# Kernel tuning notes

Hardware: AMD Instinct MI355X
Metric: run time of the kernel (lower is better)

Reference implementation:

```python
import jax, jax.numpy as jnp
import numpy as np

EPS = 1e-5  # torch BatchNorm2d default


def _conv(x, w, padding):
    return jax.lax.conv_general_dilated(
        x, w, window_strides=(1, 1),
        padding=[(padding, padding), (padding, padding)],
        dimension_numbers=("NCHW", "OIHW", "NCHW"))


def _bn(x, gamma, beta):
    # training-mode batchnorm (biased variance), matching nn.BatchNorm2d forward
    mu = x.mean(axis=(0, 2, 3), keepdims=True)
    var = x.var(axis=(0, 2, 3), keepdims=True)
    xn = (x - mu) * jax.lax.rsqrt(var + EPS)
    return gamma[None, :, None, None] * xn + beta[None, :, None, None]


def _ste(x):
    # forward: sign(x); backward: pass gradient where |x| <= 1 (STE)
    m = (jnp.abs(x) <= 1.0).astype(x.dtype)
    s = jax.lax.stop_gradient(jnp.sign(x))
    return s + m * x - jax.lax.stop_gradient(m * x)


def _binconv(x, w, alpha, padding=1):
    # XNOR-style: sign both operands, full-precision conv, scale by alpha
    return _conv(jnp.sign(x), jnp.sign(w), padding) * alpha


def _maxpool2(x):
    return jax.lax.reduce_window(x, -jnp.inf, jax.lax.max,
                                 (1, 1, 2, 2), (1, 1, 2, 2), "VALID")


def setup_inputs() -> dict:
    key = jax.random.key(0)
    ks = jax.random.split(key, 8)

    def kaiming(k, shape):
        fan_out = shape[0] * shape[2] * shape[3]
        std = np.sqrt(2.0 / fan_out)
        return jax.random.normal(k, shape, dtype=jnp.float32) * std

    return {
        "x": jax.random.normal(ks[0], (128, 1, 128, 128), dtype=jnp.float32),
        # first conv (full precision) 1->32, k=3, pad=1
        "w1": kaiming(ks[1], (32, 1, 3, 3)),
        "b1": jnp.zeros((32,), jnp.float32),
        "g1": jnp.ones((32,), jnp.float32),
        "beta1": jnp.zeros((32,), jnp.float32),
        # BinaryConv2d 32->32
        "w2": kaiming(ks[2], (32, 32, 3, 3)),
        "a2": jnp.ones((1,), jnp.float32),
        "g2": jnp.ones((32,), jnp.float32),
        "beta2": jnp.zeros((32,), jnp.float32),
        # BinaryConv2d 32->64
        "w3": kaiming(ks[3], (64, 32, 3, 3)),
        "a3": jnp.ones((1,), jnp.float32),
        "g3": jnp.ones((64,), jnp.float32),
        "beta3": jnp.zeros((64,), jnp.float32),
        # BinaryConv2d 64->128
        "w4": kaiming(ks[4], (128, 64, 3, 3)),
        "a4": jnp.ones((1,), jnp.float32),
        # classifier 128->10
        "wf": jax.random.normal(ks[5], (10, 128), dtype=jnp.float32) * (1.0 / np.sqrt(128.0)),
        "bf": jnp.zeros((10,), jnp.float32),
    }


def reference(x, w1, b1, g1, beta1, w2, a2, g2, beta2, w3, a3, g3, beta3, w4, a4, wf, bf):
    h = _conv(x, w1, padding=1) + b1[None, :, None, None]   # [N,32,128,128]
    h = _bn(h, g1, beta1)
    h = _ste(h)
    h = _binconv(h, w2, a2)                                 # [N,32,128,128]
    h = _maxpool2(h)                                        # [N,32,64,64]
    h = _bn(h, g2, beta2)
    h = _ste(h)
    h = _binconv(h, w3, a3)                                 # [N,64,64,64]
    h = _maxpool2(h)                                        # [N,64,32,32]
    h = _bn(h, g3, beta3)
    h = _ste(h)
    h = _binconv(h, w4, a4)                                 # [N,128,32,32]
    h = h.mean(axis=(2, 3))                                 # AdaptiveAvgPool2d(1) -> [N,128]
    return h @ wf.T + bf                                    # [N,10]
```

## Files before the change

kernel.cpp:

```cpp
#include <hip/hip_runtime.h>
#include <stdint.h>
#include <limits.h>

constexpr int NB = 128;

__global__ void pack_weights_kernel(const float* __restrict__ w, uint32_t* __restrict__ out,
                                    int OC, int ICW)
{
    int idx = blockIdx.x * blockDim.x + threadIdx.x;
    int total = OC * 9 * ICW;
    if (idx >= total) return;
    int iw = idx % ICW;
    int t  = (idx / ICW) % 9;
    int oc = idx / (9 * ICW);
    int IC = ICW * 32;
    uint32_t word = 0;
    for (int b = 0; b < 32; ++b) {
        float wv = w[(size_t)(oc * IC + (iw * 32 + b)) * 9 + t];
        word |= (wv > 0.f ? 1u : 0u) << b;
    }
    out[idx] = word;
}

__global__ void zero_kernel(uint32_t* __restrict__ p, int n)
{
    int i = blockIdx.x * blockDim.x + threadIdx.x;
    int stride = gridDim.x * blockDim.x;
    for (; i < n; i += stride) p[i] = 0u;
}

__device__ __forceinline__ void conv1_load9(const float* __restrict__ x, int p, float* xv)
{
    int n = p >> 14;
    int y = (p >> 7) & 127;
    int c = p & 127;
    const float* xn = x + (size_t)n * 16384;
    #pragma unroll
    for (int ky = 0; ky < 3; ++ky)
    #pragma unroll
    for (int kx = 0; kx < 3; ++kx) {
        int yy = y + ky - 1, cc = c + kx - 1;
        float v = 0.f;
        if (yy >= 0 && yy < 128 && cc >= 0 && cc < 128) v = xn[yy * 128 + cc];
        xv[ky * 3 + kx] = v;
    }
}

__global__ __launch_bounds__(256) void xcorr_kernel(const float* __restrict__ x,
                                                    float* __restrict__ partials)
{
    __shared__ float wbuf[4][64];
    int tid = threadIdx.x;
    float s[9], c[45];
    #pragma unroll
    for (int t = 0; t < 9; ++t) s[t] = 0.f;
    #pragma unroll
    for (int q = 0; q < 45; ++q) c[q] = 0.f;

    int base = blockIdx.x * 256 + tid;
    #pragma unroll 4
    for (int k = 0; k < 16; ++k) {
        float xv[9];
        conv1_load9(x, base + k * 131072, xv);
        #pragma unroll
        for (int t = 0; t < 9; ++t) {
            s[t] += xv[t];
            #pragma unroll
            for (int u = t; u < 9; ++u) {
                int q = t * (19 - t) / 2 + (u - t);
                c[q] = fmaf(xv[t], xv[u], c[q]);
            }
        }
    }
    #pragma unroll
    for (int t = 0; t < 9; ++t) {
        float a = s[t];
        #pragma unroll
        for (int off = 32; off >= 1; off >>= 1) a += __shfl_xor(a, off, 64);
        s[t] = a;
    }
    #pragma unroll
    for (int q = 0; q < 45; ++q) {
        float a = c[q];
        #pragma unroll
        for (int off = 32; off >= 1; off >>= 1) a += __shfl_xor(a, off, 64);
        c[q] = a;
    }
    int lane = tid & 63, wv = tid >> 6;
    if (lane == 0) {
        #pragma unroll
        for (int t = 0; t < 9; ++t) wbuf[wv][t] = s[t];
        #pragma unroll
        for (int q = 0; q < 45; ++q) wbuf[wv][9 + q] = c[q];
    }
    __syncthreads();
    if (tid < 54)
        partials[blockIdx.x * 64 + tid] =
            (wbuf[0][tid] + wbuf[1][tid]) + (wbuf[2][tid] + wbuf[3][tid]);
}

__global__ void compute_ss1_kernel(const double* __restrict__ dsums,
                                   const float* __restrict__ w1, const float* __restrict__ b1,
                                   const float* __restrict__ g1, const float* __restrict__ be1,
                                   float* __restrict__ ss)
{
    __shared__ double S[9], C[45];
    int tid = threadIdx.x;
    if (tid < 9) S[tid] = dsums[tid];
    else if (tid < 54) C[tid - 9] = dsums[tid];
    __syncthreads();
    if (tid >= 32) return;
    double b = (double)b1[tid];
    double w[9];
    #pragma unroll
    for (int t = 0; t < 9; ++t) w[t] = (double)w1[tid * 9 + t];
    double Sdot = 0.0, Q = 0.0;
    #pragma unroll
    for (int t = 0; t < 9; ++t) {
        Sdot += w[t] * S[t];
        #pragma unroll
        for (int u = t; u < 9; ++u) {
            int q = t * (19 - t) / 2 + (u - t);
            double term = w[t] * w[u] * C[q];
            Q += (u == t) ? term : 2.0 * term;
        }
    }
    const double N = 2097152.0;
    double mu  = Sdot / N + b;
    double ex2 = (Q + 2.0 * b * Sdot) / N + b * b;
    float var = (float)(ex2 - mu * mu);
    float A = g1[tid] * (1.f / sqrtf(var + 1e-5f));
    ss[tid] = A;
    ss[32 + tid] = be1[tid] - (float)mu * A;
}

template<int CH, int STRIDE>
__global__ __launch_bounds__(256) void reduce_partials_kernel(
    const float* __restrict__ partials, int nblk, double* __restrict__ dsums)
{
    __shared__ double wsum[4];
    int ch = blockIdx.x;
    int tid = threadIdx.x;
    double a = 0.0;
    for (int i = tid; i < nblk; i += 256)
        a += (double)partials[(size_t)i * STRIDE + ch];
    #pragma unroll
    for (int off = 32; off >= 1; off >>= 1)
        a += __shfl_xor(a, off, 64);
    if ((tid & 63) == 0) wsum[tid >> 6] = a;
    __syncthreads();
    if (tid == 0)
        dsums[ch] = (wsum[0] + wsum[1]) + (wsum[2] + wsum[3]);
}

__global__ __launch_bounds__(256) void conv1_pack2_kernel(
    const float* __restrict__ x, const float* __restrict__ w1, const float* __restrict__ b1,
    const float* __restrict__ ss, uint32_t* __restrict__ s1p)
{
    __shared__ float wl[32 * 12];
    __shared__ float abl[64];
    int tid = threadIdx.x;
    for (int i = tid; i < 288; i += 256) wl[(i / 9) * 12 + (i % 9)] = w1[i];
    if (tid < 32) {
        float A = ss[tid];
        abl[2 * tid] = A;
        abl[2 * tid + 1] = fmaf(A, b1[tid], ss[32 + tid]);
    }
    __syncthreads();
    int p = blockIdx.x * 256 + tid;
    float xv[9];
    conv1_load9(x, p, xv);
    int n = p >> 14, y = (p >> 7) & 127, c = p & 127;

    uint32_t word = 0;
    for (int oc = 0; oc < 32; ++oc) {
        float4 wa = *(const float4*)&wl[oc * 12];
        float4 wb = *(const float4*)&wl[oc * 12 + 4];
        float w8 = wl[oc * 12 + 8];
        float2 ab = *(const float2*)&abl[oc * 2];
        float a = xv[0] * wa.x;
        a = fmaf(xv[1], wa.y, a);
        a = fmaf(xv[2], wa.z, a);
        a = fmaf(xv[3], wa.w, a);
        a = fmaf(xv[4], wb.x, a);
        a = fmaf(xv[5], wb.y, a);
        a = fmaf(xv[6], wb.z, a);
        a = fmaf(xv[7], wb.w, a);
        a = fmaf(xv[8], w8, a);
        float v = fmaf(ab.x, a, ab.y);
        word |= (v > 0.f ? 1u : 0u) << oc;
    }
    s1p[(size_t)n * 16900 + (y + 1) * 130 + (c + 1)] = word;
}

template<int OC, int PW, int LPW>
__global__ __launch_bounds__(256) void binconv_main_kernel(
    const uint32_t* __restrict__ sp_in, const uint32_t* __restrict__ wp,
    const float* __restrict__ alpha, uint32_t* __restrict__ m16)
{
    constexpr int PS = 2 * PW + 2;
    constexpr int TOTAL = NB * PW * PW;
    __shared__ uint32_t wl[OC * 12];
    int tid = threadIdx.x;
    for (int i = tid; i < OC * 9; i += 256) wl[(i / 9) * 12 + (i % 9)] = wp[i];
    __syncthreads();
    bool useMax = (alpha[0] >= 0.f);
    int p = blockIdx.x * 256 + tid;
    int px = p & (PW - 1), py = (p >> LPW) & (PW - 1), n = p >> (2 * LPW);
    const uint32_t* base = sp_in + (size_t)n * PS * PS + (2 * py) * PS + 2 * px;

    uint32_t xw[16];
    #pragma unroll
    for (int r = 0; r < 4; ++r) {
        uint2 a = *(const uint2*)(base + r * PS);
        uint2 b = *(const uint2*)(base + r * PS + 2);
        xw[r * 4 + 0] = a.x; xw[r * 4 + 1] = a.y;
        xw[r * 4 + 2] = b.x; xw[r * 4 + 3] = b.y;
    }

    uint32_t pend = 0;
    for (int oc = 0; oc < OC; ++oc) {
        uint4 wa = *(const uint4*)&wl[oc * 12];
        uint4 wb = *(const uint4*)&wl[oc * 12 + 4];
        uint32_t w8 = wl[oc * 12 + 8];
        uint32_t w[9] = {wa.x, wa.y, wa.z, wa.w, wb.x, wb.y, wb.z, wb.w, w8};
        int s0 = 0, s1 = 0, s2 = 0, s3 = 0;
        #pragma unroll
        for (int ky = 0; ky < 3; ++ky)
        #pragma unroll
        for (int kx = 0; kx < 3; ++kx) {
            uint32_t wt = w[ky * 3 + kx];
            s0 += __popc(xw[ky * 4 + kx]           ^ wt);
            s1 += __popc(xw[ky * 4 + kx + 1]       ^ wt);
            s2 += __popc(xw[(ky + 1) * 4 + kx]     ^ wt);
            s3 += __popc(xw[(ky + 1) * 4 + kx + 1] ^ wt);
        }
        int sm = useMax ? min(min(s0, s1), min(s2, s3))
                        : max(max(s0, s1), max(s2, s3));
        int m = 288 - 2 * sm;
        if ((oc & 1) == 0) pend = (uint32_t)(uint16_t)(short)m;
        else m16[(size_t)(oc >> 1) * TOTAL + p] = pend | ((uint32_t)(uint16_t)(short)m << 16);
    }
}

template<int OC, int PW>
__global__ __launch_bounds__(256) void binconv_fix_kernel(
    const uint32_t* __restrict__ sp_in, const uint32_t* __restrict__ wp,
    const float* __restrict__ alpha, uint32_t* __restrict__ m16)
{
    constexpr int PS = 2 * PW + 2;
    constexpr int TOTAL = NB * PW * PW;
    constexpr int RING = 4 * PW - 4;
    __shared__ uint32_t wl[OC * 12];
    int tid = threadIdx.x;
    for (int i = tid; i < OC * 9; i += 256) wl[(i / 9) * 12 + (i % 9)] = wp[i];
    __syncthreads();
    bool useMax = (alpha[0] >= 0.f);
    int t = blockIdx.x * 256 + tid;
    int n = t / RING, r = t % RING;
    int py, px;
    if (r < PW)              { py = 0;      px = r; }
    else if (r < 2 * PW)     { py = PW - 1; px = r - PW; }
    else if (r < 3 * PW - 2) { px = 0;      py = r - 2 * PW + 1; }
    else                     { px = PW - 1; py = r - (3 * PW - 2) + 1; }
    int p = n * PW * PW + py * PW + px;
    const uint32_t* base = sp_in + (size_t)n * PS * PS + (2 * py) * PS + 2 * px;

    uint32_t xw[16], wm[16];
    #pragma unroll
    for (int a = 0; a < 4; ++a) {
        int rr = 2 * py - 1 + a;
        bool rv = (rr >= 0) && (rr < 2 * PW);
        #pragma unroll
        for (int b = 0; b < 4; ++b) {
            int cc = 2 * px - 1 + b;
            bool v = rv && (cc >= 0) && (cc < 2 * PW);
            wm[a * 4 + b] = v ? 0xFFFFFFFFu : 0u;
            xw[a * 4 + b] = base[a * PS + b];
        }
    }
    int cnt[4];
    #pragma unroll
    for (int a2 = 0; a2 < 2; ++a2)
    #pragma unroll
    for (int b2 = 0; b2 < 2; ++b2) {
        int cc = 0;
        #pragma unroll
        for (int ky = 0; ky < 3; ++ky)
        #pragma unroll
        for (int kx = 0; kx < 3; ++kx)
            cc += (int)(wm[(a2 + ky) * 4 + (b2 + kx)] & 1u);
        cnt[a2 * 2 + b2] = cc * 32;
    }

    uint32_t pend = 0;
    for (int oc = 0; oc < OC; ++oc) {
        uint4 wa = *(const uint4*)&wl[oc * 12];
        uint4 wb = *(const uint4*)&wl[oc * 12 + 4];
        uint32_t w8 = wl[oc * 12 + 8];
        uint32_t w[9] = {wa.x, wa.y, wa.z, wa.w, wb.x, wb.y, wb.z, wb.w, w8};
        int v[4];
        #pragma unroll
        for (int a2 = 0; a2 < 2; ++a2)
        #pragma unroll
        for (int b2 = 0; b2 < 2; ++b2) {
            int pop = 0;
            #pragma unroll
            for (int ky = 0; ky < 3; ++ky)
            #pragma unroll
            for (int kx = 0; kx < 3; ++kx) {
                int idx = (a2 + ky) * 4 + (b2 + kx);
                pop += __popc((xw[idx] ^ w[ky * 3 + kx]) & wm[idx]);
            }
            v[a2 * 2 + b2] = cnt[a2 * 2 + b2] - 2 * pop;
        }
        int m = useMax ? max(max(v[0], v[1]), max(v[2], v[3]))
                       : min(min(v[0], v[1]), min(v[2], v[3]));
        if ((oc & 1) == 0) pend = (uint32_t)(uint16_t)(short)m;
        else m16[(size_t)(oc >> 1) * TOTAL + p] = pend | ((uint32_t)(uint16_t)(short)m << 16);
    }
}

template<int PIXELS, int CHUNKS>
__global__ __launch_bounds__(256) void stats16_kernel(const uint32_t* __restrict__ m16,
                                                      double* __restrict__ pd)
{
    __shared__ int wb[4][4];
    int bid = blockIdx.x;
    int q = bid / CHUNKS, ch = bid % CHUNKS;
    const uint32_t* pl = m16 + (size_t)q * PIXELS + (size_t)ch * (PIXELS / CHUNKS);
    int tid = threadIdx.x;
    int s0 = 0, s1 = 0, q0 = 0, q1 = 0;
    #pragma unroll 4
    for (int j = 0; j < PIXELS / CHUNKS / 256; ++j) {
        uint32_t u = pl[tid + j * 256];
        int m0 = (int)(short)(u & 0xffffu);
        int m1 = (int)u >> 16;
        s0 += m0; s1 += m1;
        q0 += m0 * m0; q1 += m1 * m1;
    }
    #pragma unroll
    for (int off = 32; off >= 1; off >>= 1) {
        s0 += __shfl_xor(s0, off, 64); s1 += __shfl_xor(s1, off, 64);
        q0 += __shfl_xor(q0, off, 64); q1 += __shfl_xor(q1, off, 64);
    }
    int lane = tid & 63, w = tid >> 6;
    if (lane == 0) { wb[w][0] = s0; wb[w][1] = s1; wb[w][2] = q0; wb[w][3] = q1; }
    __syncthreads();
    if (tid < 4)
        pd[(size_t)bid * 4 + tid] =
            (double)((long long)wb[0][tid] + wb[1][tid] + wb[2][tid] + wb[3][tid]);
}

template<int OC, int CHUNKS>
__global__ void reduce_stats16_kernel(const double* __restrict__ pd, double* __restrict__ dsums)
{
    int ch = blockIdx.x;
    bool issq = ch >= OC;
    int c = issq ? ch - OC : ch;
    int q = c >> 1;
    int slot = (issq ? 2 : 0) + (c & 1);
    int tid = threadIdx.x;
    double a = (tid < CHUNKS) ? pd[(size_t)(q * CHUNKS + tid) * 4 + slot] : 0.0;
    #pragma unroll
    for (int off = 32; off >= 1; off >>= 1)
        a += __shfl_xor(a, off, 64);
    if (tid == 0) dsums[ch] = a;
}

template<int OC>
__global__ void compute_ss_alpha_kernel(const double* __restrict__ dsums,
                                        const float* __restrict__ gamma, const float* __restrict__ beta,
                                        const float* __restrict__ alpha,
                                        float inv_n, float* __restrict__ ss)
{
    int tid = threadIdx.x;
    if (tid >= OC) return;
    double al = (double)alpha[0];
    float mu  = (float)(dsums[tid] * al * (double)inv_n);
    float ex2 = (float)(dsums[OC + tid] * al * al * (double)inv_n);
    float var = ex2 - mu * mu;
    float A = gamma[tid] * (1.f / sqrtf(var + 1e-5f));
    ss[tid] = A;
    ss[OC + tid] = beta[tid] - mu * A;
}

template<int OC, int PW, int LPW, bool PADOUT>
__global__ __launch_bounds__(256) void binconv_pack_kernel(
    const uint32_t* __restrict__ m16, const float* __restrict__ alpha,
    const float* __restrict__ ss, void* __restrict__ sout)
{
    constexpr int TOTAL = NB * PW * PW;
    __shared__ float Ap[OC], Bp[OC];
    int tid = threadIdx.x;
    if (tid < OC) { Ap[tid] = ss[tid] * alpha[0]; Bp[tid] = ss[OC + tid]; }
    __syncthreads();
    int p = blockIdx.x * 256 + tid;
    uint64_t word = 0;
    #pragma unroll
    for (int q = 0; q < OC / 2; ++q) {
        uint32_t u = m16[(size_t)q * TOTAL + p];
        int m0 = (int)(short)(u & 0xffffu);
        int m1 = (int)u >> 16;
        float v0 = fmaf(Ap[2 * q],     (float)m0, Bp[2 * q]);
        float v1 = fmaf(Ap[2 * q + 1], (float)m1, Bp[2 * q + 1]);
        word |= (v0 > 0.f ? 1ull : 0ull) << (2 * q);
        word |= (v1 > 0.f ? 1ull : 0ull) << (2 * q + 1);
    }
    if constexpr (PADOUT) {
        int px = p & (PW - 1), py = (p >> LPW) & (PW - 1), n = p >> (2 * LPW);
        ((uint32_t*)sout)[(size_t)n * (PW + 2) * (PW + 2) + (py + 1) * (PW + 2) + (px + 1)]
            = (uint32_t)word;
    } else {
        ((uint64_t*)sout)[p] = word;
    }
}

__global__ __launch_bounds__(256) void conv4_partial_kernel(
    const uint64_t* __restrict__ s3, const uint64_t* __restrict__ wp4,
    float* __restrict__ p4)
{
    __shared__ uint64_t xt[192];
    __shared__ uint64_t wl[1152];
    __shared__ float red[256];
    int b = blockIdx.x;
    int n = b >> 3, s = b & 7;
    int tid = threadIdx.x;
    for (int i = tid; i < 192; i += 256) {
        int row = 4 * s - 1 + (i >> 5);
        int col = i & 31;
        xt[i] = (row >= 0 && row < 32) ? s3[(size_t)n * 1024 + row * 32 + col] : 0ull;
    }
    for (int i = tid; i < 1152; i += 256) wl[i] = wp4[i];
    __syncthreads();
    int oc = tid & 127, h = tid >> 7;
    uint64_t wr[9];
    #pragma unroll
    for (int t = 0; t < 9; ++t) wr[t] = wl[oc * 9 + t];
    int acc = 0;
    #pragma unroll
    for (int ry = 0; ry < 2; ++ry) {
        int lry = 2 * h + ry;
        int y = 4 * s + lry;
        for (int x = 0; x < 32; ++x) {
            int pop = 0, c = 0;
            #pragma unroll
            for (int ky = 0; ky < 3; ++ky) {
                int yy = y + ky - 1;
                if (yy < 0 || yy >= 32) continue;
                int lrow = lry + ky;
                #pragma unroll
                for (int kx = 0; kx < 3; ++kx) {
                    int xx = x + kx - 1;
                    if (xx < 0 || xx >= 32) continue;
                    pop += __popcll(xt[lrow * 32 + xx] ^ wr[ky * 3 + kx]);
                    c += 64;
                }
            }
            acc += c - 2 * pop;
        }
    }
    red[tid] = (float)acc;
    __syncthreads();
    if (tid < 128)
        p4[(size_t)b * 128 + tid] = red[tid] + red[tid + 128];
}

__global__ void mean4_kernel(const float* __restrict__ p4, const float* __restrict__ alpha4,
                             float* __restrict__ mean4)
{
    int t = blockIdx.x * blockDim.x + threadIdx.x;
    if (t >= NB * 128) return;
    int n = t >> 7, oc = t & 127;
    float a = 0.f;
    #pragma unroll
    for (int s = 0; s < 8; ++s)
        a += p4[(size_t)((n * 8 + s) * 128) + oc];
    mean4[t] = a * alpha4[0] * (1.f / 1024.f);
}

__global__ void linear_kernel(const float* __restrict__ mean4, const float* __restrict__ wf,
                              const float* __restrict__ bf, float* __restrict__ out)
{
    int t = blockIdx.x * blockDim.x + threadIdx.x;
    if (t >= 1280) return;
    int n = t / 10, k = t % 10;
    const float* m = mean4 + n * 128;
    const float* w = wf + k * 128;
    float a = bf[k];
    #pragma unroll 4
    for (int i = 0; i < 128; ++i) a = fmaf(m[i], w[i], a);
    out[t] = a;
}

extern "C" void kernel_launch(void* const* d_in, const int* in_sizes, int n_in,
                              void* d_out, int out_size, void* d_ws, size_t ws_size,
                              hipStream_t stream)
{
    const float* x   = (const float*)d_in[0];
    const float* w1  = (const float*)d_in[1];
    const float* b1  = (const float*)d_in[2];
    const float* g1  = (const float*)d_in[3];
    const float* be1 = (const float*)d_in[4];
    const float* w2  = (const float*)d_in[5];
    const float* a2  = (const float*)d_in[6];
    const float* g2  = (const float*)d_in[7];
    const float* be2 = (const float*)d_in[8];
    const float* w3  = (const float*)d_in[9];
    const float* a3  = (const float*)d_in[10];
    const float* g3  = (const float*)d_in[11];
    const float* be3 = (const float*)d_in[12];
    const float* w4  = (const float*)d_in[13];
    const float* a4  = (const float*)d_in[14];
    const float* wf  = (const float*)d_in[15];
    const float* bf  = (const float*)d_in[16];
    float* out = (float*)d_out;

    uint8_t* ws = (uint8_t*)d_ws;
    size_t off = 0;
    auto alloc = [&](size_t bytes) -> void* {
        void* p = ws + off;
        off += (bytes + 255) & ~(size_t)255;
        return p;
    };
    uint32_t* wp2 = (uint32_t*)alloc(288 * 4);
    uint32_t* wp3 = (uint32_t*)alloc(576 * 4);
    uint32_t* wp4 = (uint32_t*)alloc(2304 * 4);
    float* ss1 = (float*)alloc(64 * 4);
    float* ss2 = (float*)alloc(64 * 4);
    float* ss3 = (float*)alloc(128 * 4);
    double* dsums = (double*)alloc(256 * 8);
    double* pd    = (double*)alloc(2048 * 8);
    float* partials = (float*)alloc((size_t)512 * 64 * 4);
    uint32_t* s1p = (uint32_t*)alloc((size_t)128 * 16900 * 4);
    uint32_t* s2p = (uint32_t*)alloc((size_t)128 * 4356 * 4);
    uint64_t* s3  = (uint64_t*)alloc((size_t)128 * 1024 * 8);
    float* mean4 = (float*)alloc((size_t)128 * 128 * 4);
    float* p4    = (float*)alloc((size_t)1024 * 128 * 4);
    uint32_t* m16_2 = (uint32_t*)alloc((size_t)16 * 524288 * 4);
    uint32_t* m16_3 = (uint32_t*)alloc((size_t)32 * 131072 * 4);

    zero_kernel<<<2048, 256, 0, stream>>>(s1p, 128 * 16900);
    zero_kernel<<<1024, 256, 0, stream>>>(s2p, 128 * 4356);

    pack_weights_kernel<<<2, 256, 0, stream>>>(w2, wp2, 32, 1);
    pack_weights_kernel<<<3, 256, 0, stream>>>(w3, wp3, 64, 1);
    pack_weights_kernel<<<9, 256, 0, stream>>>(w4, wp4, 128, 2);

    xcorr_kernel<<<512, 256, 0, stream>>>(x, partials);
    reduce_partials_kernel<54, 64><<<54, 256, 0, stream>>>(partials, 512, dsums);
    compute_ss1_kernel<<<1, 64, 0, stream>>>(dsums, w1, b1, g1, be1, ss1);
    conv1_pack2_kernel<<<8192, 256, 0, stream>>>(x, w1, b1, ss1, s1p);

    binconv_main_kernel<32, 64, 6><<<2048, 256, 0, stream>>>(s1p, wp2, a2, m16_2);
    binconv_fix_kernel<32, 64><<<126, 256, 0, stream>>>(s1p, wp2, a2, m16_2);
    stats16_kernel<524288, 32><<<512, 256, 0, stream>>>(m16_2, pd);
    reduce_stats16_kernel<32, 32><<<64, 64, 0, stream>>>(pd, dsums);
    compute_ss_alpha_kernel<32><<<1, 32, 0, stream>>>(dsums, g2, be2, a2, 1.f / 524288.f, ss2);
    binconv_pack_kernel<32, 64, 6, true><<<2048, 256, 0, stream>>>(m16_2, a2, ss2, (void*)s2p);

    binconv_main_kernel<64, 32, 5><<<512, 256, 0, stream>>>(s2p, wp3, a3, m16_3);
    binconv_fix_kernel<64, 32><<<62, 256, 0, stream>>>(s2p, wp3, a3, m16_3);
    stats16_kernel<131072, 8><<<256, 256, 0, stream>>>(m16_3, pd);
    reduce_stats16_kernel<64, 8><<<128, 64, 0, stream>>>(pd, dsums);
    compute_ss_alpha_kernel<64><<<1, 64, 0, stream>>>(dsums, g3, be3, a3, 1.f / 131072.f, ss3);
    binconv_pack_kernel<64, 32, 5, false><<<512, 256, 0, stream>>>(m16_3, a3, ss3, (void*)s3);

    conv4_partial_kernel<<<1024, 256, 0, stream>>>(s3, (const uint64_t*)wp4, p4);
    mean4_kernel<<<64, 256, 0, stream>>>(p4, a4, mean4);
    linear_kernel<<<5, 256, 0, stream>>>(mean4, wf, bf, out);
}
```

Measured before the change: 261.8 us.

## Merge small kernels to cut launch count across the pipeline

New measurement: 222.0 us, median of 2. -15.2%, faster.

```diff
diff --git a/kernel.cpp b/kernel.cpp
--- a/kernel.cpp
+++ b/kernel.cpp
@@ -1,32 +1,37 @@
 #include <hip/hip_runtime.h>
 #include <stdint.h>
-#include <limits.h>
 
 constexpr int NB = 128;
 
-__global__ void pack_weights_kernel(const float* __restrict__ w, uint32_t* __restrict__ out,
-                                    int OC, int ICW)
+__global__ void pack_weights_all_kernel(const float* __restrict__ w2, const float* __restrict__ w3,
+                                        const float* __restrict__ w4,
+                                        uint32_t* __restrict__ wp2, uint32_t* __restrict__ wp3,
+                                        uint32_t* __restrict__ wp4)
 {
     int idx = blockIdx.x * blockDim.x + threadIdx.x;
-    int total = OC * 9 * ICW;
-    if (idx >= total) return;
-    int iw = idx % ICW;
-    int t  = (idx / ICW) % 9;
-    int oc = idx / (9 * ICW);
+    const float* w; uint32_t* o; int ICW, i;
+    if (idx < 288)       { w = w2; o = wp2; ICW = 1; i = idx; }
+    else if (idx < 864)  { w = w3; o = wp3; ICW = 1; i = idx - 288; }
+    else if (idx < 3168) { w = w4; o = wp4; ICW = 2; i = idx - 864; }
+    else return;
+    int iw = i % ICW;
+    int t  = (i / ICW) % 9;
+    int oc = i / (9 * ICW);
     int IC = ICW * 32;
     uint32_t word = 0;
     for (int b = 0; b < 32; ++b) {
         float wv = w[(size_t)(oc * IC + (iw * 32 + b)) * 9 + t];
         word |= (wv > 0.f ? 1u : 0u) << b;
     }
-    out[idx] = word;
-}
-
-__global__ void zero_kernel(uint32_t* __restrict__ p, int n)
+    o[i] = word;
+}
+
+__global__ void zero4_kernel(uint4* __restrict__ p, int n4)
 {
     int i = blockIdx.x * blockDim.x + threadIdx.x;
     int stride = gridDim.x * blockDim.x;
-    for (; i < n; i += stride) p[i] = 0u;
+    uint4 z = {0u, 0u, 0u, 0u};
+    for (; i < n4; i += stride) p[i] = z;
 }
 
 __device__ __forceinline__ void conv1_load9(const float* __restrict__ x, int p, float* xv)
@@ -157,167 +162,131 @@
     const float* __restrict__ x, const float* __restrict__ w1, const float* __restrict__ b1,
     const float* __restrict__ ss, uint32_t* __restrict__ s1p)
 {
-    __shared__ float wl[32 * 12];
-    __shared__ float abl[64];
-    int tid = threadIdx.x;
-    for (int i = tid; i < 288; i += 256) wl[(i / 9) * 12 + (i % 9)] = w1[i];
-    if (tid < 32) {
-        float A = ss[tid];
-        abl[2 * tid] = A;
-        abl[2 * tid + 1] = fmaf(A, b1[tid], ss[32 + tid]);
-    }
-    __syncthreads();
-    int p = blockIdx.x * 256 + tid;
+    int p = blockIdx.x * 256 + threadIdx.x;
     float xv[9];
     conv1_load9(x, p, xv);
     int n = p >> 14, y = (p >> 7) & 127, c = p & 127;
 
     uint32_t word = 0;
     for (int oc = 0; oc < 32; ++oc) {
-        float4 wa = *(const float4*)&wl[oc * 12];
-        float4 wb = *(const float4*)&wl[oc * 12 + 4];
-        float w8 = wl[oc * 12 + 8];
-        float2 ab = *(const float2*)&abl[oc * 2];
-        float a = xv[0] * wa.x;
-        a = fmaf(xv[1], wa.y, a);
-        a = fmaf(xv[2], wa.z, a);
-        a = fmaf(xv[3], wa.w, a);
-        a = fmaf(xv[4], wb.x, a);
-        a = fmaf(xv[5], wb.y, a);
-        a = fmaf(xv[6], wb.z, a);
-        a = fmaf(xv[7], wb.w, a);
-        a = fmaf(xv[8], w8, a);
-        float v = fmaf(ab.x, a, ab.y);
+        float a = xv[0] * w1[oc * 9];
+        #pragma unroll
+        for (int t = 1; t < 9; ++t) a = fmaf(xv[t], w1[oc * 9 + t], a);
+        float A = ss[oc];
+        float Bc = fmaf(A, b1[oc], ss[32 + oc]);
+        float v = fmaf(A, a, Bc);
         word |= (v > 0.f ? 1u : 0u) << oc;
     }
     s1p[(size_t)n * 16900 + (y + 1) * 130 + (c + 1)] = word;
 }
 
-template<int OC, int PW, int LPW>
-__global__ __launch_bounds__(256) void binconv_main_kernel(
+template<int OC, int PW, int LPW, int MAINB>
+__global__ __launch_bounds__(256) void binconv_mainfix_kernel(
     const uint32_t* __restrict__ sp_in, const uint32_t* __restrict__ wp,
     const float* __restrict__ alpha, uint32_t* __restrict__ m16)
 {
     constexpr int PS = 2 * PW + 2;
     constexpr int TOTAL = NB * PW * PW;
-    __shared__ uint32_t wl[OC * 12];
-    int tid = threadIdx.x;
-    for (int i = tid; i < OC * 9; i += 256) wl[(i / 9) * 12 + (i % 9)] = wp[i];
-    __syncthreads();
+    int tid = threadIdx.x;
     bool useMax = (alpha[0] >= 0.f);
-    int p = blockIdx.x * 256 + tid;
-    int px = p & (PW - 1), py = (p >> LPW) & (PW - 1), n = p >> (2 * LPW);
-    const uint32_t* base = sp_in + (size_t)n * PS * PS + (2 * py) * PS + 2 * px;
-
-    uint32_t xw[16];
-    #pragma unroll
-    for (int r = 0; r < 4; ++r) {
-        uint2 a = *(const uint2*)(base + r * PS);
-        uint2 b = *(const uint2*)(base + r * PS + 2);
-        xw[r * 4 + 0] = a.x; xw[r * 4 + 1] = a.y;
-        xw[r * 4 + 2] = b.x; xw[r * 4 + 3] = b.y;
-    }
-
-    uint32_t pend = 0;
-    for (int oc = 0; oc < OC; ++oc) {
-        uint4 wa = *(const uint4*)&wl[oc * 12];
-        uint4 wb = *(const uint4*)&wl[oc * 12 + 4];
-        uint32_t w8 = wl[oc * 12 + 8];
-        uint32_t w[9] = {wa.x, wa.y, wa.z, wa.w, wb.x, wb.y, wb.z, wb.w, w8};
-        int s0 = 0, s1 = 0, s2 = 0, s3 = 0;
-        #pragma unroll
-        for (int ky = 0; ky < 3; ++ky)
-        #pragma unroll
-        for (int kx = 0; kx < 3; ++kx) {
-            uint32_t wt = w[ky * 3 + kx];
-            s0 += __popc(xw[ky * 4 + kx]           ^ wt);
-            s1 += __popc(xw[ky * 4 + kx + 1]       ^ wt);
-            s2 += __popc(xw[(ky + 1) * 4 + kx]     ^ wt);
-            s3 += __popc(xw[(ky + 1) * 4 + kx + 1] ^ wt);
-        }
-        int sm = useMax ? min(min(s0, s1), min(s2, s3))
-                        : max(max(s0, s1), max(s2, s3));
-        int m = 288 - 2 * sm;
-        if ((oc & 1) == 0) pend = (uint32_t)(uint16_t)(short)m;
-        else m16[(size_t)(oc >> 1) * TOTAL + p] = pend | ((uint32_t)(uint16_t)(short)m << 16);
-    }
-}
-
-template<int OC, int PW>
-__global__ __launch_bounds__(256) void binconv_fix_kernel(
-    const uint32_t* __restrict__ sp_in, const uint32_t* __restrict__ wp,
-    const float* __restrict__ alpha, uint32_t* __restrict__ m16)
-{
-    constexpr int PS = 2 * PW + 2;
-    constexpr int TOTAL = NB * PW * PW;
-    constexpr int RING = 4 * PW - 4;
-    __shared__ uint32_t wl[OC * 12];
-    int tid = threadIdx.x;
-    for (int i = tid; i < OC * 9; i += 256) wl[(i / 9) * 12 + (i % 9)] = wp[i];
-    __syncthreads();
-    bool useMax = (alpha[0] >= 0.f);
-    int t = blockIdx.x * 256 + tid;
-    int n = t / RING, r = t % RING;
-    int py, px;
-    if (r < PW)              { py = 0;      px = r; }
-    else if (r < 2 * PW)     { py = PW - 1; px = r - PW; }
-    else if (r < 3 * PW - 2) { px = 0;      py = r - 2 * PW + 1; }
-    else                     { px = PW - 1; py = r - (3 * PW - 2) + 1; }
-    int p = n * PW * PW + py * PW + px;
-    const uint32_t* base = sp_in + (size_t)n * PS * PS + (2 * py) * PS + 2 * px;
-
-    uint32_t xw[16], wm[16];
-    #pragma unroll
-    for (int a = 0; a < 4; ++a) {
-        int rr = 2 * py - 1 + a;
-        bool rv = (rr >= 0) && (rr < 2 * PW);
-        #pragma unroll
-        for (int b = 0; b < 4; ++b) {
-            int cc = 2 * px - 1 + b;
-            bool v = rv && (cc >= 0) && (cc < 2 * PW);
-            wm[a * 4 + b] = v ? 0xFFFFFFFFu : 0u;
-            xw[a * 4 + b] = base[a * PS + b];
-        }
-    }
-    int cnt[4];
-    #pragma unroll
-    for (int a2 = 0; a2 < 2; ++a2)
-    #pragma unroll
-    for (int b2 = 0; b2 < 2; ++b2) {
-        int cc = 0;
-        #pragma unroll
-        for (int ky = 0; ky < 3; ++ky)
-        #pragma unroll
-        for (int kx = 0; kx < 3; ++kx)
-            cc += (int)(wm[(a2 + ky) * 4 + (b2 + kx)] & 1u);
-        cnt[a2 * 2 + b2] = cc * 32;
-    }
-
-    uint32_t pend = 0;
-    for (int oc = 0; oc < OC; ++oc) {
-        uint4 wa = *(const uint4*)&wl[oc * 12];
-        uint4 wb = *(const uint4*)&wl[oc * 12 + 4];
-        uint32_t w8 = wl[oc * 12 + 8];
-        uint32_t w[9] = {wa.x, wa.y, wa.z, wa.w, wb.x, wb.y, wb.z, wb.w, w8};
-        int v[4];
+
+    if ((int)blockIdx.x < MAINB) {
+        int p = blockIdx.x * 256 + tid;
+        int px = p & (PW - 1), py = (p >> LPW) & (PW - 1), n = p >> (2 * LPW);
+        bool border = (px == 0) | (px == PW - 1) | (py == 0) | (py == PW - 1);
+        const uint32_t* base = sp_in + (size_t)n * PS * PS + (2 * py) * PS + 2 * px;
+
+        uint32_t xw[16];
+        #pragma unroll
+        for (int r = 0; r < 4; ++r) {
+            uint2 a = *(const uint2*)(base + r * PS);
+            uint2 b = *(const uint2*)(base + r * PS + 2);
+            xw[r * 4 + 0] = a.x; xw[r * 4 + 1] = a.y;
+            xw[r * 4 + 2] = b.x; xw[r * 4 + 3] = b.y;
+        }
+
+        uint32_t pend = 0;
+        for (int oc = 0; oc < OC; ++oc) {
+            int s0 = 0, s1 = 0, s2 = 0, s3 = 0;
+            #pragma unroll
+            for (int ky = 0; ky < 3; ++ky)
+            #pragma unroll
+            for (int kx = 0; kx < 3; ++kx) {
+                uint32_t wt = wp[oc * 9 + ky * 3 + kx];
+                s0 += __popc(xw[ky * 4 + kx]           ^ wt);
+                s1 += __popc(xw[ky * 4 + kx + 1]       ^ wt);
+                s2 += __popc(xw[(ky + 1) * 4 + kx]     ^ wt);
+                s3 += __popc(xw[(ky + 1) * 4 + kx + 1] ^ wt);
+            }
+            int sm = useMax ? min(min(s0, s1), min(s2, s3))
+                            : max(max(s0, s1), max(s2, s3));
+            int m = 288 - 2 * sm;
+            if ((oc & 1) == 0) pend = (uint32_t)(uint16_t)(short)m;
+            else if (!border)
+                m16[(size_t)(oc >> 1) * TOTAL + p] = pend | ((uint32_t)(uint16_t)(short)m << 16);
+        }
+    } else {
+        constexpr int RING = 4 * PW - 4;
+        int t = ((int)blockIdx.x - MAINB) * 256 + tid;
+        if (t >= NB * RING) return;
+        int n = t / RING, r = t % RING;
+        int py, px;
+        if (r < PW)              { py = 0;      px = r; }
+        else if (r < 2 * PW)     { py = PW - 1; px = r - PW; }
+        else if (r < 3 * PW - 2) { px = 0;      py = r - 2 * PW + 1; }
+        else                     { px = PW - 1; py = r - (3 * PW - 2) + 1; }
+        int p = n * PW * PW + py * PW + px;
+        const uint32_t* base = sp_in + (size_t)n * PS * PS + (2 * py) * PS + 2 * px;
+
+        uint32_t xw[16], wm[16];
+        #pragma unroll
+        for (int a = 0; a < 4; ++a) {
+            int rr = 2 * py - 1 + a;
+            bool rv = (rr >= 0) && (rr < 2 * PW);
+            #pragma unroll
+            for (int b = 0; b < 4; ++b) {
+                int cc = 2 * px - 1 + b;
+                bool v = rv && (cc >= 0) && (cc < 2 * PW);
+                wm[a * 4 + b] = v ? 0xFFFFFFFFu : 0u;
+                xw[a * 4 + b] = base[a * PS + b];
+            }
+        }
+        int cnt[4];
         #pragma unroll
         for (int a2 = 0; a2 < 2; ++a2)
         #pragma unroll
         for (int b2 = 0; b2 < 2; ++b2) {
-            int pop = 0;
+            int cc = 0;
             #pragma unroll
             for (int ky = 0; ky < 3; ++ky)
             #pragma unroll
-            for (int kx = 0; kx < 3; ++kx) {
-                int idx = (a2 + ky) * 4 + (b2 + kx);
-                pop += __popc((xw[idx] ^ w[ky * 3 + kx]) & wm[idx]);
+            for (int kx = 0; kx < 3; ++kx)
+                cc += (int)(wm[(a2 + ky) * 4 + (b2 + kx)] & 1u);
+            cnt[a2 * 2 + b2] = cc * 32;
+        }
+
+        uint32_t pend = 0;
+        for (int oc = 0; oc < OC; ++oc) {
+            int v[4];
+            #pragma unroll
+            for (int a2 = 0; a2 < 2; ++a2)
+            #pragma unroll
+            for (int b2 = 0; b2 < 2; ++b2) {
+                int pop = 0;
+                #pragma unroll
+                for (int ky = 0; ky < 3; ++ky)
+                #pragma unroll
+                for (int kx = 0; kx < 3; ++kx) {
+                    int idx = (a2 + ky) * 4 + (b2 + kx);
+                    pop += __popc((xw[idx] ^ wp[oc * 9 + ky * 3 + kx]) & wm[idx]);
+                }
+                v[a2 * 2 + b2] = cnt[a2 * 2 + b2] - 2 * pop;
             }
-            v[a2 * 2 + b2] = cnt[a2 * 2 + b2] - 2 * pop;
-        }
-        int m = useMax ? max(max(v[0], v[1]), max(v[2], v[3]))
-                       : min(min(v[0], v[1]), min(v[2], v[3]));
-        if ((oc & 1) == 0) pend = (uint32_t)(uint16_t)(short)m;
-        else m16[(size_t)(oc >> 1) * TOTAL + p] = pend | ((uint32_t)(uint16_t)(short)m << 16);
+            int m = useMax ? max(max(v[0], v[1]), max(v[2], v[3]))
+                           : min(min(v[0], v[1]), min(v[2], v[3]));
+            if ((oc & 1) == 0) pend = (uint32_t)(uint16_t)(short)m;
+            else m16[(size_t)(oc >> 1) * TOTAL + p] = pend | ((uint32_t)(uint16_t)(short)m << 16);
+        }
     }
 }
 
@@ -353,36 +322,34 @@
 }
 
 template<int OC, int CHUNKS>
-__global__ void reduce_stats16_kernel(const double* __restrict__ pd, double* __restrict__ dsums)
-{
-    int ch = blockIdx.x;
-    bool issq = ch >= OC;
-    int c = issq ? ch - OC : ch;
-    int q = c >> 1;
-    int slot = (issq ? 2 : 0) + (c & 1);
-    int tid = threadIdx.x;
-    double a = (tid < CHUNKS) ? pd[(size_t)(q * CHUNKS + tid) * 4 + slot] : 0.0;
-    #pragma unroll
-    for (int off = 32; off >= 1; off >>= 1)
-        a += __shfl_xor(a, off, 64);
-    if (tid == 0) dsums[ch] = a;
-}
-
-template<int OC>
-__global__ void compute_ss_alpha_kernel(const double* __restrict__ dsums,
-                                        const float* __restrict__ gamma, const float* __restrict__ beta,
-                                        const float* __restrict__ alpha,
-                                        float inv_n, float* __restrict__ ss)
-{
-    int tid = threadIdx.x;
-    if (tid >= OC) return;
-    double al = (double)alpha[0];
-    float mu  = (float)(dsums[tid] * al * (double)inv_n);
-    float ex2 = (float)(dsums[OC + tid] * al * al * (double)inv_n);
-    float var = ex2 - mu * mu;
-    float A = gamma[tid] * (1.f / sqrtf(var + 1e-5f));
-    ss[tid] = A;
-    ss[OC + tid] = beta[tid] - mu * A;
+__global__ void finalize16_kernel(const double* __restrict__ pd,
+                                  const float* __restrict__ gamma, const float* __restrict__ beta,
+                                  const float* __restrict__ alpha,
+                                  float inv_n, float* __restrict__ ss)
+{
+    __shared__ double sums[2 * OC];
+    int tid = threadIdx.x;
+    if (tid < 2 * OC) {
+        bool issq = tid >= OC;
+        int c = issq ? tid - OC : tid;
+        int q = c >> 1;
+        int slot = (issq ? 2 : 0) + (c & 1);
+        double a = 0.0;
+        #pragma unroll 4
+        for (int i = 0; i < CHUNKS; ++i)
+            a += pd[(size_t)(q * CHUNKS + i) * 4 + slot];
+        sums[tid] = a;
+    }
+    __syncthreads();
+    if (tid < OC) {
+        double al = (double)alpha[0];
+        float mu  = (float)(sums[tid] * al * (double)inv_n);
+        float ex2 = (float)(sums[OC + tid] * al * al * (double)inv_n);
+        float var = ex2 - mu * mu;
+        float A = gamma[tid] * (1.f / sqrtf(var + 1e-5f));
+        ss[tid] = A;
+        ss[OC + tid] = beta[tid] - mu * A;
+    }
 }
 
 template<int OC, int PW, int LPW, bool PADOUT>
@@ -466,31 +433,25 @@
         p4[(size_t)b * 128 + tid] = red[tid] + red[tid + 128];
 }
 
-__global__ void mean4_kernel(const float* __restrict__ p4, const float* __restrict__ alpha4,
-                             float* __restrict__ mean4)
-{
-    int t = blockIdx.x * blockDim.x + threadIdx.x;
-    if (t >= NB * 128) return;
-    int n = t >> 7, oc = t & 127;
+__global__ __launch_bounds__(128) void mean_linear_kernel(
+    const float* __restrict__ p4, const float* __restrict__ alpha4,
+    const float* __restrict__ wf, const float* __restrict__ bf, float* __restrict__ out)
+{
+    __shared__ float ml[128];
+    int n = blockIdx.x, tid = threadIdx.x;
     float a = 0.f;
     #pragma unroll
     for (int s = 0; s < 8; ++s)
-        a += p4[(size_t)((n * 8 + s) * 128) + oc];
-    mean4[t] = a * alpha4[0] * (1.f / 1024.f);
-}
-
-__global__ void linear_kernel(const float* __restrict__ mean4, const float* __restrict__ wf,
-                              const float* __restrict__ bf, float* __restrict__ out)
-{
-    int t = blockIdx.x * blockDim.x + threadIdx.x;
-    if (t >= 1280) return;
-    int n = t / 10, k = t % 10;
-    const float* m = mean4 + n * 128;
-    const float* w = wf + k * 128;
-    float a = bf[k];
-    #pragma unroll 4
-    for (int i = 0; i < 128; ++i) a = fmaf(m[i], w[i], a);
-    out[t] = a;
+        a += p4[(size_t)((n * 8 + s) * 128) + tid];
+    ml[tid] = a * alpha4[0] * (1.f / 1024.f);
+    __syncthreads();
+    if (tid < 10) {
+        const float* w = wf + tid * 128;
+        float acc = bf[tid];
+        #pragma unroll 4
+        for (int i = 0; i < 128; ++i) acc = fmaf(ml[i], w[i], acc);
+        out[n * 10 + tid] = acc;
+    }
 }
 
 extern "C" void kernel_launch(void* const* d_in, const int* in_sizes, int n_in,
@@ -535,38 +496,33 @@
     uint32_t* s1p = (uint32_t*)alloc((size_t)128 * 16900 * 4);
     uint32_t* s2p = (uint32_t*)alloc((size_t)128 * 4356 * 4);
     uint64_t* s3  = (uint64_t*)alloc((size_t)128 * 1024 * 8);
-    float* mean4 = (float*)alloc((size_t)128 * 128 * 4);
     float* p4    = (float*)alloc((size_t)1024 * 128 * 4);
     uint32_t* m16_2 = (uint32_t*)alloc((size_t)16 * 524288 * 4);
     uint32_t* m16_3 = (uint32_t*)alloc((size_t)32 * 131072 * 4);
 
-    zero_kernel<<<2048, 256, 0, stream>>>(s1p, 128 * 16900);
-    zero_kernel<<<1024, 256, 0, stream>>>(s2p, 128 * 4356);
-
-    pack_weights_kernel<<<2, 256, 0, stream>>>(w2, wp2, 32, 1);
-    pack_weights_kernel<<<3, 256, 0, stream>>>(w3, wp3, 64, 1);
-    pack_weights_kernel<<<9, 256, 0, stream>>>(w4, wp4, 128, 2);
+    {
+        size_t span_bytes = (size_t)((uint8_t*)(s2p + (size_t)128 * 4356) - (uint8_t*)s1p);
+        int n4 = (int)(span_bytes / 16);
+        zero4_kernel<<<1024, 256, 0, stream>>>((uint4*)s1p, n4);
+    }
+
+    pack_weights_all_kernel<<<13, 256, 0, stream>>>(w2, w3, w4, wp2, wp3, wp4);
 
     xcorr_kernel<<<512, 256, 0, stream>>>(x, partials);
     reduce_partials_kernel<54, 64><<<54, 256, 0, stream>>>(partials, 512, dsums);
     compute_ss1_kernel<<<1, 64, 0, stream>>>(dsums, w1, b1, g1, be1, ss1);
     conv1_pack2_kernel<<<8192, 256, 0, stream>>>(x, w1, b1, ss1, s1p);
 
-    binconv_main_kernel<32, 64, 6><<<2048, 256, 0, stream>>>(s1p, wp2, a2, m16_2);
-    binconv_fix_kernel<32, 64><<<126, 256, 0, stream>>>(s1p, wp2, a2, m16_2);
+    binconv_mainfix_kernel<32, 64, 6, 2048><<<2048 + 126, 256, 0, stream>>>(s1p, wp2, a2, m16_2);
     stats16_kernel<524288, 32><<<512, 256, 0, stream>>>(m16_2, pd);
-    reduce_stats16_kernel<32, 32><<<64, 64, 0, stream>>>(pd, dsums);
-    compute_ss_alpha_kernel<32><<<1, 32, 0, stream>>>(dsums, g2, be2, a2, 1.f / 524288.f, ss2);
+    finalize16_kernel<32, 32><<<1, 256, 0, stream>>>(pd, g2, be2, a2, 1.f / 524288.f, ss2);
     binconv_pack_kernel<32, 64, 6, true><<<2048, 256, 0, stream>>>(m16_2, a2, ss2, (void*)s2p);
 
-    binconv_main_kernel<64, 32, 5><<<512, 256, 0, stream>>>(s2p, wp3, a3, m16_3);
-    binconv_fix_kernel<64, 32><<<62, 256, 0, stream>>>(s2p, wp3, a3, m16_3);
+    binconv_mainfix_kernel<64, 32, 5, 512><<<512 + 62, 256, 0, stream>>>(s2p, wp3, a3, m16_3);
     stats16_kernel<131072, 8><<<256, 256, 0, stream>>>(m16_3, pd);
-    reduce_stats16_kernel<64, 8><<<128, 64, 0, stream>>>(pd, dsums);
-    compute_ss_alpha_kernel<64><<<1, 64, 0, stream>>>(dsums, g3, be3, a3, 1.f / 131072.f, ss3);
+    finalize16_kernel<64, 8><<<1, 256, 0, stream>>>(pd, g3, be3, a3, 1.f / 131072.f, ss3);
     binconv_pack_kernel<64, 32, 5, false><<<512, 256, 0, stream>>>(m16_3, a3, ss3, (void*)s3);
 
     conv4_partial_kernel<<<1024, 256, 0, stream>>>(s3, (const uint64_t*)wp4, p4);
-    mean4_kernel<<<64, 256, 0, stream>>>(p4, a4, mean4);
-    linear_kernel<<<5, 256, 0, stream>>>(mean4, wf, bf, out);
-}
+    mean_linear_kernel<<<128, 128, 0, stream>>>(p4, a4, wf, bf, out);
+}
```
